# Performance work log

Measured on AMD Instinct MI355X. Metric: run time of the kernel, lower is better.

Reference implementation:

```python
import jax, jax.numpy as jnp
import numpy as np

V = np.array([[1.0, 1.0, 1.0], [1.0, -1.0, 1.0], [1.0, 1.0, -1.0]], dtype=np.float32)


def _lin_combs(kernels: np.ndarray) -> np.ndarray:
    """Project (O, C, 3, 3) kernels onto inverse of the 9x9 GCK +/-1 basis.
    Returns (O, C*9) with layout c*9 + (3*i + j), matching the torch module."""
    O, C = kernels.shape[0], kernels.shape[1]
    # basis_flat[k=3i+j, p=3r+s] = V[i,r] * V[j,s]
    basis_flat = np.einsum('ir,js->ijrs', V, V).reshape(9, 9)
    basis_inv = np.linalg.inv(basis_flat)
    kflat = kernels.reshape(O, C, 9)
    comb = np.einsum('kp,ocp->ock', basis_inv, kflat)  # (O, C, 9)
    return np.ascontiguousarray(comb.reshape(O, C * 9))


def setup_inputs() -> dict:
    key = jax.random.key(0)
    k1, k2 = jax.random.split(key)
    B, C, O, H, W = 1, 64, 64, 514, 514
    x = jax.random.normal(k1, (B, C, H, W), dtype=jnp.float32)
    kernels = np.asarray(jax.random.normal(k2, (O, C, 3, 3), dtype=jnp.float32))
    linCombs = jnp.asarray(_lin_combs(kernels))  # (O, C*9)
    return {"input": x, "linCombs": linCombs}


def reference(input, linCombs):
    # GCK 3x3 conv: rowwise +/-1 stage -> colwise +/-1 stage -> linComb matmul.
    x = input
    B, C, H, W = x.shape
    O = linCombs.shape[0]
    Ho, Wo = H - 2, W - 2  # padding = 0
    Vj = jnp.asarray(V)
    # rowwise stage: convolve (cross-correlate) along rows with each +/-1 vector
    rows = jnp.stack([x[:, :, r:r + Ho, :] for r in range(3)])       # (3,B,C,Ho,W)
    rowwise = jnp.einsum('ir,rbchw->bcihw', Vj, rows)                 # (B,C,3,Ho,W)
    # colwise stage: convolve along columns with each +/-1 vector
    cols = jnp.stack([rowwise[..., s:s + Wo] for s in range(3)])      # (3,B,C,3,Ho,Wo)
    colwise = jnp.einsum('js,sbcihw->bcijhw', Vj, cols)               # (B,C,3,3,Ho,Wo)
    feats = colwise.reshape(B, C * 9, Ho * Wo)                        # k = c*9 + 3i + j
    out = jnp.einsum('ok,bkp->bop', linCombs, feats)
    return out.reshape(B, O, Ho, Wo)
```

## Files before the change

kernel.cpp:

```cpp
#include <hip/hip_runtime.h>
#include <hip/hip_bf16.h>


constexpr int kC = 64, kO = 64;
constexpr int kH = 514, kW = 514;
constexpr int kHO = 512, kWO = 512;
constexpr int kNPIX = kH * kW;
constexpr int LCOLS = 66;

typedef __attribute__((ext_vector_type(8))) short short8;
typedef __attribute__((ext_vector_type(4))) float floatx4;

__device__ inline unsigned short f2bf(float f) {
    unsigned int u = __float_as_uint(f);
    unsigned int r = (u + 0x7fffu + ((u >> 16) & 1u)) >> 16;
    return (unsigned short)r;
}

__global__ void gck_wprep(const float* __restrict__ lin, unsigned short* __restrict__ w2) {
    int t = blockIdx.x * 256 + threadIdx.x;
    if (t >= kO * kC * 9) return;
    int tap = t % 9;
    int c   = (t / 9) % kC;
    int o   = t / (9 * kC);
    int r = tap / 3, s = tap % 3;
    const float Vm[3][3] = {{1.f, 1.f, 1.f}, {1.f, -1.f, 1.f}, {1.f, 1.f, -1.f}};
    float acc = 0.f;
#pragma unroll
    for (int i = 0; i < 3; i++)
#pragma unroll
        for (int j = 0; j < 3; j++)
            acc += lin[o * (kC * 9) + c * 9 + 3 * i + j] * Vm[i][r] * Vm[j][s];
    int kglob = tap * 64 + c;
    int ks = kglob >> 5, kg = (kglob >> 3) & 3, e = kglob & 7;
    w2[((ks * 4 + kg) * 64 + o) * 8 + e] = f2bf(acc);
}

__global__ __launch_bounds__(256, 4) void gck_conv(const float* __restrict__ x,
                                                   const unsigned short* __restrict__ w2,
                                                   float* __restrict__ out) {
    __shared__ unsigned short xs[4 * LCOLS * 64];

    const int bid = blockIdx.x;
    const int ct = bid & 7;
    const int rt = bid >> 3;
    const int hbase = rt * 2;
    const int wbase = ct * 64;
    const int t    = threadIdx.x;
    const int wave = t >> 6;
    const int lane = t & 63;
    const int l16  = lane & 15;
    const int kg   = lane >> 4;
    const int hw   = wave >> 1;
    const int o0   = (wave & 1) * 32;

    {
        const int cp  = t & 31;
        const int cg  = t >> 5;
        const int ch0 = cg * 8;
        const int colb = cp * 2;
#pragma unroll
        for (int r = 0; r < 4; ++r) {
            const float* gp = x + (size_t)(hbase + r) * kW + wbase + colb;
            float2 f[8];
#pragma unroll
            for (int c = 0; c < 8; ++c)
                f[c] = *reinterpret_cast<const float2*>(gp + (size_t)(ch0 + c) * kNPIX);
#pragma unroll
            for (int j = 0; j < 2; ++j) {
                int col = colb + j;
                short8 u8;
#pragma unroll
                for (int c = 0; c < 8; ++c) u8[c] = (short)f2bf(j ? f[c].y : f[c].x);
                int swz = (cg ^ (col & 7) ^ ((col >> 3) & 7)) & 7;
                *reinterpret_cast<short8*>(&xs[(r * LCOLS + col) * 64 + swz * 8]) = u8;
            }
        }
#pragma unroll
        for (int j = 0; j < 2; ++j) {
            int idx = j * 256 + t;
            int col = 64 + (idx & 1);
            int ch  = (idx >> 1) & 63;
            int r   = idx >> 7;
            float f = x[(size_t)ch * kNPIX + (size_t)(hbase + r) * kW + wbase + col];
            int swz = ((ch >> 3) ^ (col & 7) ^ ((col >> 3) & 7)) & 7;
            xs[(r * LCOLS + col) * 64 + swz * 8 + (ch & 7)] = f2bf(f);
        }
    }
    __syncthreads();

    floatx4 acc[2][4];
#pragma unroll
    for (int m = 0; m < 2; m++)
#pragma unroll
        for (int n = 0; n < 4; n++) acc[m][n] = (floatx4){0.f, 0.f, 0.f, 0.f};

    const short8* w2v = reinterpret_cast<const short8*>(w2);

    short8 a_cur[2];
#pragma unroll
    for (int m = 0; m < 2; m++) a_cur[m] = w2v[(0 * 4 + kg) * 64 + o0 + m * 16 + l16];

#pragma unroll 2
    for (int ks = 0; ks < 18; ++ks) {
        int tap = ks >> 1;
        int r0  = tap / 3;
        int s   = tap - r0 * 3;

        short8 a_nxt[2];
        int ksn = (ks < 17) ? ks + 1 : ks;
#pragma unroll
        for (int m = 0; m < 2; m++) a_nxt[m] = w2v[(ksn * 4 + kg) * 64 + o0 + m * 16 + l16];

        int rr = hw + r0;
        int u  = (ks & 1) * 4 + kg;
        short8 b[4];
#pragma unroll
        for (int n = 0; n < 4; ++n) {
            int col  = n * 16 + l16 + s;
            int swz  = (u ^ (col & 7) ^ ((col >> 3) & 7)) & 7;
            b[n] = *reinterpret_cast<const short8*>(&xs[(rr * LCOLS + col) * 64 + swz * 8]);
        }

#pragma unroll
        for (int m = 0; m < 2; m++)
#pragma unroll
            for (int n = 0; n < 4; n++)
                acc[m][n] = __builtin_amdgcn_mfma_f32_16x16x32_bf16(a_cur[m], b[n], acc[m][n], 0, 0, 0);

#pragma unroll
        for (int m = 0; m < 2; m++) a_cur[m] = a_nxt[m];
    }

    const int h = hbase + hw;
#pragma unroll
    for (int m = 0; m < 2; m++) {
#pragma unroll
        for (int n = 0; n < 4; n++) {
            int wcol = wbase + n * 16 + l16;
#pragma unroll
            for (int j = 0; j < 4; j++) {
                int o = o0 + m * 16 + kg * 4 + j;
                out[((size_t)o * kHO + h) * kWO + wcol] = acc[m][n][j];
            }
        }
    }
}

extern "C" void kernel_launch(void* const* d_in, const int* in_sizes, int n_in,
                              void* d_out, int out_size, void* d_ws, size_t ws_size,
                              hipStream_t stream) {
    const float* x   = (const float*)d_in[0];
    const float* lin = (const float*)d_in[1];
    float* out = (float*)d_out;

    unsigned short* w2 = (unsigned short*)d_ws;

    gck_wprep<<<(kO * kC * 9 + 255) / 256, 256, 0, stream>>>(lin, w2);
    gck_conv<<<(kHO / 2) * 8, 256, 0, stream>>>(x, w2, out);
}
```

Before: 142.2 us.

## Widen conv tile to 128 columns with 512 threads and XCD-aware block mapping

Each block now covers 2 output rows by 128 columns using 8 waves instead of 64 columns with 4 waves. This halves the halo overhead per block in the LDS input staging. Each wave now computes all 64 output channels for 32 pixels rather than 32 channels for 64 pixels, which changes the balance between weight loads and LDS input reads. Block indices are remapped so that neighbouring blocks on the same XCD share row ranges, improving L2 locality. In exchange, blocks use twice the LDS and more accumulator registers, which may reduce occupancy.

```diff
diff --git a/kernel.cpp b/kernel.cpp
--- a/kernel.cpp
+++ b/kernel.cpp
@@ -6,7 +6,7 @@
 constexpr int kH = 514, kW = 514;
 constexpr int kHO = 512, kWO = 512;
 constexpr int kNPIX = kH * kW;
-constexpr int LCOLS = 66;
+constexpr int LCOLS = 130;
 
 typedef __attribute__((ext_vector_type(8))) short short8;
 typedef __attribute__((ext_vector_type(4))) float floatx4;
@@ -36,52 +36,48 @@
     w2[((ks * 4 + kg) * 64 + o) * 8 + e] = f2bf(acc);
 }
 
-__global__ __launch_bounds__(256, 4) void gck_conv(const float* __restrict__ x,
+__global__ __launch_bounds__(512, 4) void gck_conv(const float* __restrict__ x,
                                                    const unsigned short* __restrict__ w2,
                                                    float* __restrict__ out) {
     __shared__ unsigned short xs[4 * LCOLS * 64];
 
     const int bid = blockIdx.x;
-    const int ct = bid & 7;
-    const int rt = bid >> 3;
+    const int xcd = bid & 7;
+    const int ct  = xcd & 3;
+    const int rt  = (xcd >> 2) * 128 + (bid >> 3);
     const int hbase = rt * 2;
-    const int wbase = ct * 64;
+    const int wbase = ct * 128;
     const int t    = threadIdx.x;
     const int wave = t >> 6;
     const int lane = t & 63;
     const int l16  = lane & 15;
     const int kg   = lane >> 4;
-    const int hw   = wave >> 1;
-    const int o0   = (wave & 1) * 32;
 
     {
-        const int cp  = t & 31;
-        const int cg  = t >> 5;
-        const int ch0 = cg * 8;
-        const int colb = cp * 2;
+        const int cp  = t & 63;
+        const int u   = t >> 6;
+        const int ch0 = u * 8;
 #pragma unroll
         for (int r = 0; r < 4; ++r) {
-            const float* gp = x + (size_t)(hbase + r) * kW + wbase + colb;
+            const float* gp = x + (size_t)(hbase + r) * kW + wbase + cp * 2;
             float2 f[8];
 #pragma unroll
-            for (int c = 0; c < 8; ++c)
-                f[c] = *reinterpret_cast<const float2*>(gp + (size_t)(ch0 + c) * kNPIX);
+            for (int e = 0; e < 8; ++e)
+                f[e] = *reinterpret_cast<const float2*>(gp + (size_t)(ch0 + e) * kNPIX);
 #pragma unroll
             for (int j = 0; j < 2; ++j) {
-                int col = colb + j;
+                int col = cp * 2 + j;
                 short8 u8;
 #pragma unroll
-                for (int c = 0; c < 8; ++c) u8[c] = (short)f2bf(j ? f[c].y : f[c].x);
-                int swz = (cg ^ (col & 7) ^ ((col >> 3) & 7)) & 7;
+                for (int e = 0; e < 8; ++e) u8[e] = (short)f2bf(j ? f[e].y : f[e].x);
+                int swz = (u ^ (col & 7) ^ ((col >> 3) & 7)) & 7;
                 *reinterpret_cast<short8*>(&xs[(r * LCOLS + col) * 64 + swz * 8]) = u8;
             }
         }
-#pragma unroll
-        for (int j = 0; j < 2; ++j) {
-            int idx = j * 256 + t;
-            int col = 64 + (idx & 1);
-            int ch  = (idx >> 1) & 63;
-            int r   = idx >> 7;
+        {
+            int col = 128 + (t & 1);
+            int ch  = (t >> 1) & 63;
+            int r   = t >> 7;
             float f = x[(size_t)ch * kNPIX + (size_t)(hbase + r) * kW + wbase + col];
             int swz = ((ch >> 3) ^ (col & 7) ^ ((col >> 3) & 7)) & 7;
             xs[(r * LCOLS + col) * 64 + swz * 8 + (ch & 7)] = f2bf(f);
@@ -89,17 +85,20 @@
     }
     __syncthreads();
 
-    floatx4 acc[2][4];
+    const int hw  = wave >> 2;
+    const int px0 = (wave & 3) * 32;
+
+    floatx4 acc[4][2];
 #pragma unroll
-    for (int m = 0; m < 2; m++)
+    for (int m = 0; m < 4; m++)
 #pragma unroll
-        for (int n = 0; n < 4; n++) acc[m][n] = (floatx4){0.f, 0.f, 0.f, 0.f};
+        for (int n = 0; n < 2; n++) acc[m][n] = (floatx4){0.f, 0.f, 0.f, 0.f};
 
     const short8* w2v = reinterpret_cast<const short8*>(w2);
 
-    short8 a_cur[2];
+    short8 a_cur[4];
 #pragma unroll
-    for (int m = 0; m < 2; m++) a_cur[m] = w2v[(0 * 4 + kg) * 64 + o0 + m * 16 + l16];
+    for (int m = 0; m < 4; m++) a_cur[m] = w2v[(0 * 4 + kg) * 64 + m * 16 + l16];
 
 #pragma unroll 2
     for (int ks = 0; ks < 18; ++ks) {
@@ -107,40 +106,40 @@
         int r0  = tap / 3;
         int s   = tap - r0 * 3;
 
-        short8 a_nxt[2];
+        short8 a_nxt[4];
         int ksn = (ks < 17) ? ks + 1 : ks;
 #pragma unroll
-        for (int m = 0; m < 2; m++) a_nxt[m] = w2v[(ksn * 4 + kg) * 64 + o0 + m * 16 + l16];
+        for (int m = 0; m < 4; m++) a_nxt[m] = w2v[(ksn * 4 + kg) * 64 + m * 16 + l16];
 
         int rr = hw + r0;
-        int u  = (ks & 1) * 4 + kg;
-        short8 b[4];
+        int u2 = (ks & 1) * 4 + kg;
+        short8 b[2];
 #pragma unroll
-        for (int n = 0; n < 4; ++n) {
-            int col  = n * 16 + l16 + s;
-            int swz  = (u ^ (col & 7) ^ ((col >> 3) & 7)) & 7;
+        for (int n = 0; n < 2; ++n) {
+            int col = px0 + n * 16 + l16 + s;
+            int swz = (u2 ^ (col & 7) ^ ((col >> 3) & 7)) & 7;
             b[n] = *reinterpret_cast<const short8*>(&xs[(rr * LCOLS + col) * 64 + swz * 8]);
         }
 
 #pragma unroll
-        for (int m = 0; m < 2; m++)
+        for (int m = 0; m < 4; m++)
 #pragma unroll
-            for (int n = 0; n < 4; n++)
+            for (int n = 0; n < 2; n++)
                 acc[m][n] = __builtin_amdgcn_mfma_f32_16x16x32_bf16(a_cur[m], b[n], acc[m][n], 0, 0, 0);
 
 #pragma unroll
-        for (int m = 0; m < 2; m++) a_cur[m] = a_nxt[m];
+        for (int m = 0; m < 4; m++) a_cur[m] = a_nxt[m];
     }
 
     const int h = hbase + hw;
 #pragma unroll
-    for (int m = 0; m < 2; m++) {
+    for (int m = 0; m < 4; m++) {
 #pragma unroll
-        for (int n = 0; n < 4; n++) {
-            int wcol = wbase + n * 16 + l16;
+        for (int n = 0; n < 2; n++) {
+            int wcol = wbase + px0 + n * 16 + l16;
 #pragma unroll
             for (int j = 0; j < 4; j++) {
-                int o = o0 + m * 16 + kg * 4 + j;
+                int o = m * 16 + kg * 4 + j;
                 out[((size_t)o * kHO + h) * kWO + wcol] = acc[m][n][j];
             }
         }
@@ -157,5 +156,5 @@
     unsigned short* w2 = (unsigned short*)d_ws;
 
     gck_wprep<<<(kO * kC * 9 + 255) / 256, 256, 0, stream>>>(lin, w2);
-    gck_conv<<<(kHO / 2) * 8, 256, 0, stream>>>(x, w2, out);
+    gck_conv<<<1024, 512, 0, stream>>>(x, w2, out);
 }
```

Measured after the change: 143.1 us. No clear change (+0.6%).
